# Kernel optimization log

Hardware: AMD Instinct MI355X
Metric: run time of the kernel (lower is better)

The kernel has to match this reference:

```python
import jax, jax.numpy as jnp
import numpy as np

D_MODEL = 1024
H = 16
D_K = D_MODEL // H
EPS = 1e-8


def _feature_map(x):
    # elu(x) + 1 (Performer/linear-attention positive feature map)
    return jax.nn.elu(x) + 1.0


def setup_inputs() -> dict:
    key = jax.random.key(0)
    ks = jax.random.split(key, 8)
    B, L = 4, 2048
    q = jax.random.normal(ks[0], (B, L, D_MODEL), dtype=jnp.float32)
    k = jax.random.normal(ks[1], (B, L, D_MODEL), dtype=jnp.float32)
    v = jax.random.normal(ks[2], (B, L, D_MODEL), dtype=jnp.float32)
    mask = jnp.ones((B, 1, 1, L), dtype=bool)
    s = 1.0 / np.sqrt(D_MODEL)
    w_q = jax.random.normal(ks[3], (D_MODEL, D_MODEL), dtype=jnp.float32) * s
    w_k = jax.random.normal(ks[4], (D_MODEL, D_MODEL), dtype=jnp.float32) * s
    w_v = jax.random.normal(ks[5], (D_MODEL, D_MODEL), dtype=jnp.float32) * s
    w_o = jax.random.normal(ks[6], (D_MODEL, D_MODEL), dtype=jnp.float32) * s
    return {"q": q, "k": k, "v": v, "mask": mask,
            "w_q": w_q, "w_k": w_k, "w_v": w_v, "w_o": w_o}


def reference(q, k, v, mask, w_q, w_k, w_v, w_o):
    # Linear (use_Linear=True) branch of MultiHeadAttentionBlock.forward.
    B, Lq, _ = q.shape
    Lk = k.shape[1]
    # fused-style projections (torch Linear: x @ W.T), split into heads -> bhnd
    query = (q @ w_q.T).reshape(B, Lq, H, D_K).transpose(0, 2, 1, 3)
    key_  = (k @ w_k.T).reshape(B, Lk, H, D_K).transpose(0, 2, 1, 3)
    value = (v @ w_v.T).reshape(B, Lk, H, D_K).transpose(0, 2, 1, 3)

    Q = _feature_map(query)            # [B,H,Lq,d_k]
    K = _feature_map(key_)             # [B,H,Lk,d_k]
    KV = jnp.einsum('bhnd,bhnm->bhdm', K, value)           # [B,H,d_k,d_k]
    Z = 1.0 / (jnp.einsum('bhnd,bhd->bhn', Q, K.sum(axis=2)) + EPS)  # [B,H,Lq]
    out = jnp.einsum('bhnd,bhdm,bhn->bhnm', Q, KV, Z)      # [B,H,Lq,d_k]

    out = out.transpose(0, 2, 1, 3).reshape(B, Lq, D_MODEL)
    return out @ w_o.T
```

## Files before the change

### kernel.cpp

```cpp
#include <hip/hip_runtime.h>
#include <cstdint>
#include <cstddef>

typedef __bf16 bf16;
typedef __bf16 bf16x8 __attribute__((ext_vector_type(8)));
typedef __bf16 bf16x4 __attribute__((ext_vector_type(4)));
typedef float  f32x4  __attribute__((ext_vector_type(4)));

#define DM     1024
#define MROWS  8192
#define LSEQ   2048
#define NHEAD  16
#define BHEADS 64
#define KV_S   16
#define KVT_STRIDE 4160

__device__ __forceinline__ void async16(const void* g, void* l) {
    __builtin_amdgcn_global_load_lds(
        (const __attribute__((address_space(1))) void*)g,
        (__attribute__((address_space(3))) void*)l, 16, 0, 0);
}

struct CastArgs {
    const float* s[7];
    bf16*        d[7];
    int          n4[7];
};

__global__ __launch_bounds__(256) void cast_all(CastArgs a) {
    const int z = blockIdx.z;
    const int n4 = a.n4[z];
    const float* __restrict__ s = a.s[z];
    bf16* __restrict__ d = a.d[z];
    for (int i = blockIdx.x * 256 + threadIdx.x; i < n4; i += 1024 * 256) {
        float4 f = ((const float4*)s)[i];
        bf16x4 o; o[0] = (bf16)f.x; o[1] = (bf16)f.y; o[2] = (bf16)f.z; o[3] = (bf16)f.w;
        ((bf16x4*)d)[i] = o;
    }
}

struct GemmArgs {
    const bf16* A[3];
    const bf16* B[3];
    void*       C[3];
    int         mode[3];
};

__global__ __launch_bounds__(256, 3) void gemm_nt(GemmArgs args) {
    const int z = blockIdx.z;
    const bf16* __restrict__ A  = args.A[z];
    const bf16* __restrict__ Bm = args.B[z];
    void* Cp = args.C[z];
    const int mode = args.mode[z];
    const int K = DM;

    __shared__ __attribute__((aligned(16))) bf16 sA[128 * 64];
    __shared__ __attribute__((aligned(16))) bf16 sB[128 * 64];

    const int tid  = threadIdx.x;
    const int wave = tid >> 6;
    const int lane = tid & 63;
    const int wm = wave >> 1, wn = wave & 1;

    const int fb = blockIdx.x + 8 * (int)blockIdx.y;
    const int bx = (fb >> 3) & 7;
    const int by = (fb & 7) * 8 + (fb >> 6);
    const int row0 = by * 128;
    const int col0 = bx * 128;

    const int rr = lane >> 3;
    const int cc = lane & 7;
    const int csw = ((cc ^ rr) * 8);
    const bf16* gA = A  + (size_t)(row0 + wave * 32 + rr) * K + csw;
    const bf16* gB = Bm + (size_t)(col0 + wave * 32 + rr) * K + csw;

    f32x4 acc[4][4] = {};

    const int lr = lane & 15;
    const int qd = lane >> 4;
    const int swz = lr & 7;

    for (int k0 = 0; k0 < K; k0 += 64) {
        #pragma unroll
        for (int j = 0; j < 4; ++j) {
            async16(gA + k0 + (size_t)(j * 8) * K, &sA[(wave * 32 + j * 8) * 64]);
            async16(gB + k0 + (size_t)(j * 8) * K, &sB[(wave * 32 + j * 8) * 64]);
        }
        __syncthreads();

        #pragma unroll
        for (int ks = 0; ks < 2; ++ks) {
            bf16x8 af[4], bfr[4];
            #pragma unroll
            for (int mi = 0; mi < 4; ++mi)
                af[mi] = *(const bf16x8*)&sA[(wm * 64 + mi * 16 + lr) * 64 + (((ks * 4 + qd) ^ swz) * 8)];
            #pragma unroll
            for (int ni = 0; ni < 4; ++ni)
                bfr[ni] = *(const bf16x8*)&sB[(wn * 64 + ni * 16 + lr) * 64 + (((ks * 4 + qd) ^ swz) * 8)];
            #pragma unroll
            for (int mi = 0; mi < 4; ++mi)
                #pragma unroll
                for (int ni = 0; ni < 4; ++ni)
                    acc[mi][ni] = __builtin_amdgcn_mfma_f32_16x16x32_bf16(af[mi], bfr[ni], acc[mi][ni], 0, 0, 0);
        }
        __syncthreads();
    }

    if (mode >= 3) {
        #pragma unroll
        for (int mi = 0; mi < 4; ++mi) {
            const int grow0 = row0 + wm * 64 + mi * 16 + qd * 4;
            const int b  = grow0 >> 11;
            const int n0 = grow0 & 2047;
            #pragma unroll
            for (int ni = 0; ni < 4; ++ni) {
                const int gcol = col0 + wn * 64 + ni * 16 + lr;
                const int h = gcol >> 6;
                const int d = gcol & 63;
                bf16x4 o;
                #pragma unroll
                for (int r = 0; r < 4; ++r) {
                    float val = acc[mi][ni][r];
                    if (mode == 4) val = (val > 0.f) ? (val + 1.f) : __expf(val);
                    o[r] = (bf16)val;
                }
                *(bf16x4*)&((bf16*)Cp)[(size_t)((b * 16 + h) * 64 + d) * 2048 + n0] = o;
            }
        }
    } else {
        #pragma unroll
        for (int mi = 0; mi < 4; ++mi) {
            #pragma unroll
            for (int ni = 0; ni < 4; ++ni) {
                #pragma unroll
                for (int r = 0; r < 4; ++r) {
                    const int grow = row0 + wm * 64 + mi * 16 + qd * 4 + r;
                    const int gcol = col0 + wn * 64 + ni * 16 + lr;
                    float val = acc[mi][ni][r];
                    if (mode == 1) val = (val > 0.f) ? (val + 1.f) : __expf(val);
                    ((bf16*)Cp)[(size_t)grow * DM + gcol] = (bf16)val;
                }
            }
        }
    }
}

__global__ __launch_bounds__(256, 4) void gemm_fin(const bf16* __restrict__ A,
                                                   const bf16* __restrict__ Bm,
                                                   float* __restrict__ C) {
    const int K = DM;
    __shared__ __attribute__((aligned(16))) bf16 sA[128 * 64];
    __shared__ __attribute__((aligned(16))) bf16 sB[64 * 64];

    const int tid  = threadIdx.x;
    const int wave = tid >> 6;
    const int lane = tid & 63;
    const int wm = wave >> 1, wn = wave & 1;

    const int fb = blockIdx.x + 16 * (int)blockIdx.y;
    const int xcd = fb & 7;
    const int g = fb >> 3;
    const int bx = g & 15;
    const int by = xcd * 8 + (g >> 4);
    const int row0 = by * 128;
    const int col0 = bx * 64;

    const int rr = lane >> 3;
    const int cc = lane & 7;
    const int csw = ((cc ^ rr) * 8);
    const bf16* gA = A  + (size_t)(row0 + wave * 32 + rr) * K + csw;
    const bf16* gB = Bm + (size_t)(col0 + wave * 16 + rr) * K + csw;

    f32x4 acc[4][2] = {};

    const int lr = lane & 15;
    const int qd = lane >> 4;
    const int swz = lr & 7;

    for (int k0 = 0; k0 < K; k0 += 64) {
        #pragma unroll
        for (int j = 0; j < 4; ++j)
            async16(gA + k0 + (size_t)(j * 8) * K, &sA[(wave * 32 + j * 8) * 64]);
        #pragma unroll
        for (int j = 0; j < 2; ++j)
            async16(gB + k0 + (size_t)(j * 8) * K, &sB[(wave * 16 + j * 8) * 64]);
        __syncthreads();

        #pragma unroll
        for (int ks = 0; ks < 2; ++ks) {
            bf16x8 af[4], bfr[2];
            #pragma unroll
            for (int mi = 0; mi < 4; ++mi)
                af[mi] = *(const bf16x8*)&sA[(wm * 64 + mi * 16 + lr) * 64 + (((ks * 4 + qd) ^ swz) * 8)];
            #pragma unroll
            for (int ni = 0; ni < 2; ++ni)
                bfr[ni] = *(const bf16x8*)&sB[(wn * 32 + ni * 16 + lr) * 64 + (((ks * 4 + qd) ^ swz) * 8)];
            #pragma unroll
            for (int mi = 0; mi < 4; ++mi)
                #pragma unroll
                for (int ni = 0; ni < 2; ++ni)
                    acc[mi][ni] = __builtin_amdgcn_mfma_f32_16x16x32_bf16(af[mi], bfr[ni], acc[mi][ni], 0, 0, 0);
        }
        __syncthreads();
    }

    #pragma unroll
    for (int mi = 0; mi < 4; ++mi)
        #pragma unroll
        for (int ni = 0; ni < 2; ++ni)
            #pragma unroll
            for (int r = 0; r < 4; ++r) {
                const int grow = row0 + wm * 64 + mi * 16 + qd * 4 + r;
                const int gcol = col0 + wn * 32 + ni * 16 + lr;
                C[(size_t)grow * DM + gcol] = acc[mi][ni][r];
            }
}

__global__ __launch_bounds__(256, 4) void kv_mfma(const bf16* __restrict__ KpT,
                                                  const bf16* __restrict__ VpT,
                                                  float* __restrict__ KVTp) {
    const int bh = blockIdx.x, s = blockIdx.y;
    const int tid = threadIdx.x, wave = tid >> 6, lane = tid & 63;

    __shared__ __attribute__((aligned(16))) bf16 sVT[64 * 128];
    __shared__ __attribute__((aligned(16))) bf16 sKT[64 * 128];

    #pragma unroll
    for (int j = 0; j < 4; ++j) {
        const int r  = wave * 16 + j * 4 + (lane >> 4);
        const int cg = (lane & 15) ^ (r & 7);
        const size_t gofs = (size_t)(bh * 64 + r) * 2048 + s * 128 + cg * 8;
        async16(VpT + gofs, &sVT[(wave * 16 + j * 4) * 128]);
        async16(KpT + gofs, &sKT[(wave * 16 + j * 4) * 128]);
    }
    __syncthreads();

    const int lr = lane & 15, qd = lane >> 4;
    f32x4 acc[4] = {};
    const int rA = wave * 16 + lr;
    #pragma unroll
    for (int k0 = 0; k0 < 4; ++k0) {
        const int ch = k0 * 4 + qd;
        bf16x8 a = *(const bf16x8*)&sVT[rA * 128 + ((ch ^ (rA & 7)) * 8)];
        #pragma unroll
        for (int ni = 0; ni < 4; ++ni) {
            const int rB = ni * 16 + lr;
            bf16x8 b = *(const bf16x8*)&sKT[rB * 128 + ((ch ^ (rB & 7)) * 8)];
            acc[ni] = __builtin_amdgcn_mfma_f32_16x16x32_bf16(a, b, acc[ni], 0, 0, 0);
        }
    }

    float* outp = &KVTp[(size_t)(bh * KV_S + s) * KVT_STRIDE];
    #pragma unroll
    for (int ni = 0; ni < 4; ++ni)
        #pragma unroll
        for (int r = 0; r < 4; ++r)
            outp[(wave * 16 + qd * 4 + r) * 64 + ni * 16 + lr] = acc[ni][r];

    if (wave == 0) {
        float ks = 0.f;
        #pragma unroll
        for (int c2 = 0; c2 < 16; ++c2) {
            bf16x8 kk = *(const bf16x8*)&sKT[lane * 128 + ((c2 ^ (lane & 7)) * 8)];
            #pragma unroll
            for (int j = 0; j < 8; ++j) ks += (float)kk[j];
        }
        outp[4096 + lane] = ks;
    }
}

__global__ __launch_bounds__(256) void kv_reduce(const float* __restrict__ KVTp,
                                                 bf16* __restrict__ KVT,
                                                 float* __restrict__ Ksum) {
    const int bh = blockIdx.x;
    const int idx = blockIdx.y * 256 + threadIdx.x;
    if (idx >= KVT_STRIDE) return;
    float s = 0.f;
    #pragma unroll
    for (int p = 0; p < KV_S; ++p) s += KVTp[(size_t)(bh * KV_S + p) * KVT_STRIDE + idx];
    if (idx < 4096) KVT[(size_t)bh * 4096 + idx] = (bf16)s;
    else            Ksum[bh * 64 + (idx - 4096)] = s;
}

__global__ __launch_bounds__(256, 4) void attn_out(const bf16* __restrict__ Qp,
                                                   const bf16* __restrict__ KVT,
                                                   const float* __restrict__ Ksum,
                                                   bf16* __restrict__ Ab) {
    const int bh = blockIdx.y;
    const int b = bh >> 4, h = bh & 15;
    const int row0 = blockIdx.x * 128;
    const int tid = threadIdx.x, wave = tid >> 6, lane = tid & 63;

    __shared__ __attribute__((aligned(16))) bf16 sQ[128 * 64];
    __shared__ __attribute__((aligned(16))) bf16 sKV[64 * 64];
    __shared__ float sKs[64];

    const int rr8 = lane >> 3;
    const int cc8 = lane & 7;
    const int csw = ((cc8 ^ rr8) * 8);

    const bf16* qbase = &Qp[(size_t)(b * LSEQ + row0) * DM + h * 64];
    #pragma unroll
    for (int j = 0; j < 4; ++j) {
        const int r0 = wave * 32 + j * 8;
        async16(qbase + (size_t)(r0 + rr8) * DM + csw, &sQ[r0 * 64]);
    }
    const bf16* kvbase = &KVT[(size_t)bh * 4096];
    #pragma unroll
    for (int j = 0; j < 2; ++j) {
        const int r0 = wave * 16 + j * 8;
        async16(kvbase + (r0 + rr8) * 64 + csw, &sKV[r0 * 64]);
    }
    if (tid < 64) sKs[tid] = Ksum[bh * 64 + tid];
    __syncthreads();

    const int zrow = lane >> 1;
    const int dh = lane & 1;
    float zacc = 0.f;
    {
        const bf16* qr = &sQ[(wave * 32 + zrow) * 64];
        #pragma unroll
        for (int c = 0; c < 4; ++c) {
            const int chunk = dh * 4 + c;
            bf16x8 q8 = *(const bf16x8*)&qr[(chunk ^ (zrow & 7)) * 8];
            const float* ksp = &sKs[chunk * 8];
            #pragma unroll
            for (int j = 0; j < 8; ++j) zacc += (float)q8[j] * ksp[j];
        }
    }
    zacc += __shfl_xor(zacc, 1, 64);
    const float zinv = 1.0f / (zacc + 1e-8f);

    f32x4 acc[2][4] = {};
    const int lr = lane & 15, qd = lane >> 4;
    const int swz = lr & 7;
    #pragma unroll
    for (int ks = 0; ks < 2; ++ks) {
        bf16x8 af[2], bfr[4];
        #pragma unroll
        for (int mi = 0; mi < 2; ++mi)
            af[mi] = *(const bf16x8*)&sQ[(wave * 32 + mi * 16 + lr) * 64 + (((ks * 4 + qd) ^ swz) * 8)];
        #pragma unroll
        for (int ni = 0; ni < 4; ++ni)
            bfr[ni] = *(const bf16x8*)&sKV[(ni * 16 + lr) * 64 + (((ks * 4 + qd) ^ swz) * 8)];
        #pragma unroll
        for (int mi = 0; mi < 2; ++mi)
            #pragma unroll
            for (int ni = 0; ni < 4; ++ni)
                acc[mi][ni] = __builtin_amdgcn_mfma_f32_16x16x32_bf16(af[mi], bfr[ni], acc[mi][ni], 0, 0, 0);
    }

    #pragma unroll
    for (int mi = 0; mi < 2; ++mi) {
        #pragma unroll
        for (int rr = 0; rr < 4; ++rr) {
            const int rlocal = mi * 16 + qd * 4 + rr;
            const float zv = __shfl(zinv, rlocal * 2, 64);
            const int nrow = row0 + wave * 32 + rlocal;
            #pragma unroll
            for (int ni = 0; ni < 4; ++ni)
                Ab[(size_t)(b * LSEQ + nrow) * DM + h * 64 + ni * 16 + lr] =
                    (bf16)(acc[mi][ni][rr] * zv);
        }
    }
}

extern "C" void kernel_launch(void* const* d_in, const int* in_sizes, int n_in,
                              void* d_out, int out_size, void* d_ws, size_t ws_size,
                              hipStream_t stream) {
    const float* q  = (const float*)d_in[0];
    const float* k  = (const float*)d_in[1];
    const float* v  = (const float*)d_in[2];
    const float* wq = (const float*)d_in[4];
    const float* wk = (const float*)d_in[5];
    const float* wv = (const float*)d_in[6];
    const float* wo = (const float*)d_in[7];

    char* ws = (char*)d_ws;
    size_t off = 0;
    auto alloc = [&](size_t bytes) -> void* {
        void* p = ws + off;
        off += (bytes + 255) & ~(size_t)255;
        return p;
    };

    bf16* qb   = (bf16*)alloc((size_t)MROWS * DM * 2);
    bf16* kb   = (bf16*)alloc((size_t)MROWS * DM * 2);
    bf16* vb   = (bf16*)alloc((size_t)MROWS * DM * 2);
    bf16* wqb  = (bf16*)alloc((size_t)DM * DM * 2);
    bf16* wkb  = (bf16*)alloc((size_t)DM * DM * 2);
    bf16* wvb  = (bf16*)alloc((size_t)DM * DM * 2);
    bf16* wob  = (bf16*)alloc((size_t)DM * DM * 2);
    bf16* Qp   = (bf16*)alloc((size_t)MROWS * DM * 2);
    bf16* KpT  = (bf16*)alloc((size_t)MROWS * DM * 2);
    bf16* VpT  = (bf16*)alloc((size_t)MROWS * DM * 2);
    bf16* Ab   = (bf16*)alloc((size_t)MROWS * DM * 2);
    float* KVTp = (float*)alloc((size_t)BHEADS * KV_S * KVT_STRIDE * 4);
    bf16* KVT  = (bf16*)alloc((size_t)BHEADS * 4096 * 2);
    float* Ksum = (float*)alloc((size_t)BHEADS * 64 * 4);

    CastArgs ca;
    ca.s[0] = q;  ca.s[1] = k;  ca.s[2] = v;  ca.s[3] = wq; ca.s[4] = wk; ca.s[5] = wv; ca.s[6] = wo;
    ca.d[0] = qb; ca.d[1] = kb; ca.d[2] = vb; ca.d[3] = wqb; ca.d[4] = wkb; ca.d[5] = wvb; ca.d[6] = wob;
    const int n4_big = MROWS * DM / 4, n4_w = DM * DM / 4;
    ca.n4[0] = n4_big; ca.n4[1] = n4_big; ca.n4[2] = n4_big;
    ca.n4[3] = n4_w; ca.n4[4] = n4_w; ca.n4[5] = n4_w; ca.n4[6] = n4_w;
    cast_all<<<dim3(1024, 1, 7), 256, 0, stream>>>(ca);

    GemmArgs pa;
    pa.A[0] = qb;  pa.A[1] = kb;  pa.A[2] = vb;
    pa.B[0] = wqb; pa.B[1] = wkb; pa.B[2] = wvb;
    pa.C[0] = Qp;  pa.C[1] = KpT; pa.C[2] = VpT;
    pa.mode[0] = 1; pa.mode[1] = 4; pa.mode[2] = 3;
    gemm_nt<<<dim3(DM / 128, MROWS / 128, 3), 256, 0, stream>>>(pa);

    kv_mfma<<<dim3(BHEADS, KV_S), 256, 0, stream>>>(KpT, VpT, KVTp);
    kv_reduce<<<dim3(BHEADS, (KVT_STRIDE + 255) / 256), 256, 0, stream>>>(KVTp, KVT, Ksum);

    attn_out<<<dim3(LSEQ / 128, BHEADS), 256, 0, stream>>>(Qp, KVT, Ksum, Ab);

    gemm_fin<<<dim3(DM / 64, MROWS / 128), 256, 0, stream>>>(Ab, wob, (float*)d_out);
}
```

Before: 256.6 us.

## Fuse fp32-to-bf16 activation cast into projection GEMM and enlarge output GEMM tile

```diff
diff --git a/kernel.cpp b/kernel.cpp
--- a/kernel.cpp
+++ b/kernel.cpp
@@ -22,40 +22,35 @@
 }
 
 struct CastArgs {
-    const float* s[7];
-    bf16*        d[7];
-    int          n4[7];
+    const float* s[4];
+    bf16*        d[4];
 };
 
-__global__ __launch_bounds__(256) void cast_all(CastArgs a) {
+__global__ __launch_bounds__(256) void cast_w(CastArgs a) {
     const int z = blockIdx.z;
-    const int n4 = a.n4[z];
-    const float* __restrict__ s = a.s[z];
-    bf16* __restrict__ d = a.d[z];
-    for (int i = blockIdx.x * 256 + threadIdx.x; i < n4; i += 1024 * 256) {
-        float4 f = ((const float4*)s)[i];
-        bf16x4 o; o[0] = (bf16)f.x; o[1] = (bf16)f.y; o[2] = (bf16)f.z; o[3] = (bf16)f.w;
-        ((bf16x4*)d)[i] = o;
-    }
+    const int i = blockIdx.x * 256 + threadIdx.x;
+    float4 f = ((const float4*)a.s[z])[i];
+    bf16x4 o; o[0] = (bf16)f.x; o[1] = (bf16)f.y; o[2] = (bf16)f.z; o[3] = (bf16)f.w;
+    ((bf16x4*)a.d[z])[i] = o;
 }
 
 struct GemmArgs {
-    const bf16* A[3];
-    const bf16* B[3];
-    void*       C[3];
-    int         mode[3];
+    const float* A[3];
+    const bf16*  B[3];
+    void*        C[3];
+    int          mode[3];
 };
 
 __global__ __launch_bounds__(256, 3) void gemm_nt(GemmArgs args) {
     const int z = blockIdx.z;
-    const bf16* __restrict__ A  = args.A[z];
-    const bf16* __restrict__ Bm = args.B[z];
+    const float* __restrict__ A  = args.A[z];
+    const bf16*  __restrict__ Bm = args.B[z];
     void* Cp = args.C[z];
     const int mode = args.mode[z];
     const int K = DM;
 
-    __shared__ __attribute__((aligned(16))) bf16 sA[128 * 64];
-    __shared__ __attribute__((aligned(16))) bf16 sB[128 * 64];
+    __shared__ __attribute__((aligned(16))) float sAf[128 * 64];
+    __shared__ __attribute__((aligned(16))) bf16  sB[128 * 64];
 
     const int tid  = threadIdx.x;
     const int wave = tid >> 6;
@@ -68,11 +63,12 @@
     const int row0 = by * 128;
     const int col0 = bx * 128;
 
-    const int rr = lane >> 3;
-    const int cc = lane & 7;
-    const int csw = ((cc ^ rr) * 8);
-    const bf16* gA = A  + (size_t)(row0 + wave * 32 + rr) * K + csw;
-    const bf16* gB = Bm + (size_t)(col0 + wave * 32 + rr) * K + csw;
+    const int rr4  = lane >> 4;
+    const int cc16 = lane & 15;
+    const int rr8 = lane >> 3;
+    const int cc8 = lane & 7;
+    const int cswB = ((cc8 ^ rr8) * 8);
+    const bf16* gB = Bm + (size_t)(col0 + wave * 32 + rr8) * K + cswB;
 
     f32x4 acc[4][4] = {};
 
@@ -82,18 +78,30 @@
 
     for (int k0 = 0; k0 < K; k0 += 64) {
         #pragma unroll
-        for (int j = 0; j < 4; ++j) {
-            async16(gA + k0 + (size_t)(j * 8) * K, &sA[(wave * 32 + j * 8) * 64]);
+        for (int j = 0; j < 8; ++j) {
+            const int rl = wave * 32 + j * 4 + rr4;
+            const int g  = cc16 ^ (rl & 7);
+            async16(A + (size_t)(row0 + rl) * K + k0 + g * 4, &sAf[(wave * 32 + j * 4) * 64]);
+        }
+        #pragma unroll
+        for (int j = 0; j < 4; ++j)
             async16(gB + k0 + (size_t)(j * 8) * K, &sB[(wave * 32 + j * 8) * 64]);
-        }
         __syncthreads();
 
         #pragma unroll
         for (int ks = 0; ks < 2; ++ks) {
             bf16x8 af[4], bfr[4];
             #pragma unroll
-            for (int mi = 0; mi < 4; ++mi)
-                af[mi] = *(const bf16x8*)&sA[(wm * 64 + mi * 16 + lr) * 64 + (((ks * 4 + qd) ^ swz) * 8)];
+            for (int mi = 0; mi < 4; ++mi) {
+                const int row = wm * 64 + mi * 16 + lr;
+                const int c0 = (ks * 4 + qd) * 2;
+                f32x4 lo = *(const f32x4*)&sAf[row * 64 + ((c0 ^ swz) * 4)];
+                f32x4 hi = *(const f32x4*)&sAf[row * 64 + (((c0 + 1) ^ swz) * 4)];
+                bf16x8 t;
+                t[0] = (bf16)lo[0]; t[1] = (bf16)lo[1]; t[2] = (bf16)lo[2]; t[3] = (bf16)lo[3];
+                t[4] = (bf16)hi[0]; t[5] = (bf16)hi[1]; t[6] = (bf16)hi[2]; t[7] = (bf16)hi[3];
+                af[mi] = t;
+            }
             #pragma unroll
             for (int ni = 0; ni < 4; ++ni)
                 bfr[ni] = *(const bf16x8*)&sB[(wn * 64 + ni * 16 + lr) * 64 + (((ks * 4 + qd) ^ swz) * 8)];
@@ -145,33 +153,31 @@
     }
 }
 
-__global__ __launch_bounds__(256, 4) void gemm_fin(const bf16* __restrict__ A,
+__global__ __launch_bounds__(256, 3) void gemm_fin(const bf16* __restrict__ A,
                                                    const bf16* __restrict__ Bm,
                                                    float* __restrict__ C) {
     const int K = DM;
     __shared__ __attribute__((aligned(16))) bf16 sA[128 * 64];
-    __shared__ __attribute__((aligned(16))) bf16 sB[64 * 64];
+    __shared__ __attribute__((aligned(16))) bf16 sB[128 * 64];
 
     const int tid  = threadIdx.x;
     const int wave = tid >> 6;
     const int lane = tid & 63;
     const int wm = wave >> 1, wn = wave & 1;
 
-    const int fb = blockIdx.x + 16 * (int)blockIdx.y;
-    const int xcd = fb & 7;
-    const int g = fb >> 3;
-    const int bx = g & 15;
-    const int by = xcd * 8 + (g >> 4);
+    const int fb = blockIdx.x + 8 * (int)blockIdx.y;
+    const int bx = (fb >> 3) & 7;
+    const int by = (fb & 7) * 8 + (fb >> 6);
     const int row0 = by * 128;
-    const int col0 = bx * 64;
+    const int col0 = bx * 128;
 
     const int rr = lane >> 3;
     const int cc = lane & 7;
     const int csw = ((cc ^ rr) * 8);
     const bf16* gA = A  + (size_t)(row0 + wave * 32 + rr) * K + csw;
-    const bf16* gB = Bm + (size_t)(col0 + wave * 16 + rr) * K + csw;
-
-    f32x4 acc[4][2] = {};
+    const bf16* gB = Bm + (size_t)(col0 + wave * 32 + rr) * K + csw;
+
+    f32x4 acc[4][4] = {};
 
     const int lr = lane & 15;
     const int qd = lane >> 4;
@@ -179,26 +185,25 @@
 
     for (int k0 = 0; k0 < K; k0 += 64) {
         #pragma unroll
-        for (int j = 0; j < 4; ++j)
+        for (int j = 0; j < 4; ++j) {
             async16(gA + k0 + (size_t)(j * 8) * K, &sA[(wave * 32 + j * 8) * 64]);
-        #pragma unroll
-        for (int j = 0; j < 2; ++j)
-            async16(gB + k0 + (size_t)(j * 8) * K, &sB[(wave * 16 + j * 8) * 64]);
+            async16(gB + k0 + (size_t)(j * 8) * K, &sB[(wave * 32 + j * 8) * 64]);
+        }
         __syncthreads();
 
         #pragma unroll
         for (int ks = 0; ks < 2; ++ks) {
-            bf16x8 af[4], bfr[2];
+            bf16x8 af[4], bfr[4];
             #pragma unroll
             for (int mi = 0; mi < 4; ++mi)
                 af[mi] = *(const bf16x8*)&sA[(wm * 64 + mi * 16 + lr) * 64 + (((ks * 4 + qd) ^ swz) * 8)];
             #pragma unroll
-            for (int ni = 0; ni < 2; ++ni)
-                bfr[ni] = *(const bf16x8*)&sB[(wn * 32 + ni * 16 + lr) * 64 + (((ks * 4 + qd) ^ swz) * 8)];
+            for (int ni = 0; ni < 4; ++ni)
+                bfr[ni] = *(const bf16x8*)&sB[(wn * 64 + ni * 16 + lr) * 64 + (((ks * 4 + qd) ^ swz) * 8)];
             #pragma unroll
             for (int mi = 0; mi < 4; ++mi)
                 #pragma unroll
-                for (int ni = 0; ni < 2; ++ni)
+                for (int ni = 0; ni < 4; ++ni)
                     acc[mi][ni] = __builtin_amdgcn_mfma_f32_16x16x32_bf16(af[mi], bfr[ni], acc[mi][ni], 0, 0, 0);
         }
         __syncthreads();
@@ -207,11 +212,11 @@
     #pragma unroll
     for (int mi = 0; mi < 4; ++mi)
         #pragma unroll
-        for (int ni = 0; ni < 2; ++ni)
+        for (int ni = 0; ni < 4; ++ni)
             #pragma unroll
             for (int r = 0; r < 4; ++r) {
                 const int grow = row0 + wm * 64 + mi * 16 + qd * 4 + r;
-                const int gcol = col0 + wn * 32 + ni * 16 + lr;
+                const int gcol = col0 + wn * 64 + ni * 16 + lr;
                 C[(size_t)grow * DM + gcol] = acc[mi][ni][r];
             }
 }
@@ -384,9 +389,6 @@
         return p;
     };
 
-    bf16* qb   = (bf16*)alloc((size_t)MROWS * DM * 2);
-    bf16* kb   = (bf16*)alloc((size_t)MROWS * DM * 2);
-    bf16* vb   = (bf16*)alloc((size_t)MROWS * DM * 2);
     bf16* wqb  = (bf16*)alloc((size_t)DM * DM * 2);
     bf16* wkb  = (bf16*)alloc((size_t)DM * DM * 2);
     bf16* wvb  = (bf16*)alloc((size_t)DM * DM * 2);
@@ -400,15 +402,12 @@
     float* Ksum = (float*)alloc((size_t)BHEADS * 64 * 4);
 
     CastArgs ca;
-    ca.s[0] = q;  ca.s[1] = k;  ca.s[2] = v;  ca.s[3] = wq; ca.s[4] = wk; ca.s[5] = wv; ca.s[6] = wo;
-    ca.d[0] = qb; ca.d[1] = kb; ca.d[2] = vb; ca.d[3] = wqb; ca.d[4] = wkb; ca.d[5] = wvb; ca.d[6] = wob;
-    const int n4_big = MROWS * DM / 4, n4_w = DM * DM / 4;
-    ca.n4[0] = n4_big; ca.n4[1] = n4_big; ca.n4[2] = n4_big;
-    ca.n4[3] = n4_w; ca.n4[4] = n4_w; ca.n4[5] = n4_w; ca.n4[6] = n4_w;
-    cast_all<<<dim3(1024, 1, 7), 256, 0, stream>>>(ca);
+    ca.s[0] = wq;  ca.s[1] = wk;  ca.s[2] = wv;  ca.s[3] = wo;
+    ca.d[0] = wqb; ca.d[1] = wkb; ca.d[2] = wvb; ca.d[3] = wob;
+    cast_w<<<dim3(DM * DM / 4 / 256, 1, 4), 256, 0, stream>>>(ca);
 
     GemmArgs pa;
-    pa.A[0] = qb;  pa.A[1] = kb;  pa.A[2] = vb;
+    pa.A[0] = q;   pa.A[1] = k;   pa.A[2] = v;
     pa.B[0] = wqb; pa.B[1] = wkb; pa.B[2] = wvb;
     pa.C[0] = Qp;  pa.C[1] = KpT; pa.C[2] = VpT;
     pa.mode[0] = 1; pa.mode[1] = 4; pa.mode[2] = 3;
@@ -419,5 +418,5 @@
 
     attn_out<<<dim3(LSEQ / 128, BHEADS), 256, 0, stream>>>(Qp, KVT, Ksum, Ab);
 
-    gemm_fin<<<dim3(DM / 64, MROWS / 128), 256, 0, stream>>>(Ab, wob, (float*)d_out);
-}
+    gemm_fin<<<dim3(DM / 128, MROWS / 128), 256, 0, stream>>>(Ab, wob, (float*)d_out);
+}
```

Result: slower. 269.5 us (+5.0%).

## Enlarge output GEMM tile to 128x128 and halve KV split partials in bf16

Applied to the files above, without the earlier changes.

```diff
diff --git a/kernel.cpp b/kernel.cpp
--- a/kernel.cpp
+++ b/kernel.cpp
@@ -12,8 +12,7 @@
 #define LSEQ   2048
 #define NHEAD  16
 #define BHEADS 64
-#define KV_S   16
-#define KVT_STRIDE 4160
+#define KV_S   8
 
 __device__ __forceinline__ void async16(const void* g, void* l) {
     __builtin_amdgcn_global_load_lds(
@@ -145,33 +144,31 @@
     }
 }
 
-__global__ __launch_bounds__(256, 4) void gemm_fin(const bf16* __restrict__ A,
+__global__ __launch_bounds__(256, 3) void gemm_fin(const bf16* __restrict__ A,
                                                    const bf16* __restrict__ Bm,
                                                    float* __restrict__ C) {
     const int K = DM;
     __shared__ __attribute__((aligned(16))) bf16 sA[128 * 64];
-    __shared__ __attribute__((aligned(16))) bf16 sB[64 * 64];
+    __shared__ __attribute__((aligned(16))) bf16 sB[128 * 64];
 
     const int tid  = threadIdx.x;
     const int wave = tid >> 6;
     const int lane = tid & 63;
     const int wm = wave >> 1, wn = wave & 1;
 
-    const int fb = blockIdx.x + 16 * (int)blockIdx.y;
-    const int xcd = fb & 7;
-    const int g = fb >> 3;
-    const int bx = g & 15;
-    const int by = xcd * 8 + (g >> 4);
+    const int fb = blockIdx.x + 8 * (int)blockIdx.y;
+    const int bx = (fb >> 3) & 7;
+    const int by = (fb & 7) * 8 + (fb >> 6);
     const int row0 = by * 128;
-    const int col0 = bx * 64;
+    const int col0 = bx * 128;
 
     const int rr = lane >> 3;
     const int cc = lane & 7;
     const int csw = ((cc ^ rr) * 8);
     const bf16* gA = A  + (size_t)(row0 + wave * 32 + rr) * K + csw;
-    const bf16* gB = Bm + (size_t)(col0 + wave * 16 + rr) * K + csw;
-
-    f32x4 acc[4][2] = {};
+    const bf16* gB = Bm + (size_t)(col0 + wave * 32 + rr) * K + csw;
+
+    f32x4 acc[4][4] = {};
 
     const int lr = lane & 15;
     const int qd = lane >> 4;
@@ -179,26 +176,25 @@
 
     for (int k0 = 0; k0 < K; k0 += 64) {
         #pragma unroll
-        for (int j = 0; j < 4; ++j)
+        for (int j = 0; j < 4; ++j) {
             async16(gA + k0 + (size_t)(j * 8) * K, &sA[(wave * 32 + j * 8) * 64]);
-        #pragma unroll
-        for (int j = 0; j < 2; ++j)
-            async16(gB + k0 + (size_t)(j * 8) * K, &sB[(wave * 16 + j * 8) * 64]);
+            async16(gB + k0 + (size_t)(j * 8) * K, &sB[(wave * 32 + j * 8) * 64]);
+        }
         __syncthreads();
 
         #pragma unroll
         for (int ks = 0; ks < 2; ++ks) {
-            bf16x8 af[4], bfr[2];
+            bf16x8 af[4], bfr[4];
             #pragma unroll
             for (int mi = 0; mi < 4; ++mi)
                 af[mi] = *(const bf16x8*)&sA[(wm * 64 + mi * 16 + lr) * 64 + (((ks * 4 + qd) ^ swz) * 8)];
             #pragma unroll
-            for (int ni = 0; ni < 2; ++ni)
-                bfr[ni] = *(const bf16x8*)&sB[(wn * 32 + ni * 16 + lr) * 64 + (((ks * 4 + qd) ^ swz) * 8)];
+            for (int ni = 0; ni < 4; ++ni)
+                bfr[ni] = *(const bf16x8*)&sB[(wn * 64 + ni * 16 + lr) * 64 + (((ks * 4 + qd) ^ swz) * 8)];
             #pragma unroll
             for (int mi = 0; mi < 4; ++mi)
                 #pragma unroll
-                for (int ni = 0; ni < 2; ++ni)
+                for (int ni = 0; ni < 4; ++ni)
                     acc[mi][ni] = __builtin_amdgcn_mfma_f32_16x16x32_bf16(af[mi], bfr[ni], acc[mi][ni], 0, 0, 0);
         }
         __syncthreads();
@@ -207,79 +203,91 @@
     #pragma unroll
     for (int mi = 0; mi < 4; ++mi)
         #pragma unroll
-        for (int ni = 0; ni < 2; ++ni)
+        for (int ni = 0; ni < 4; ++ni)
             #pragma unroll
             for (int r = 0; r < 4; ++r) {
                 const int grow = row0 + wm * 64 + mi * 16 + qd * 4 + r;
-                const int gcol = col0 + wn * 32 + ni * 16 + lr;
+                const int gcol = col0 + wn * 64 + ni * 16 + lr;
                 C[(size_t)grow * DM + gcol] = acc[mi][ni][r];
             }
 }
 
 __global__ __launch_bounds__(256, 4) void kv_mfma(const bf16* __restrict__ KpT,
                                                   const bf16* __restrict__ VpT,
-                                                  float* __restrict__ KVTp) {
+                                                  bf16* __restrict__ KVTp,
+                                                  float* __restrict__ KsumP) {
     const int bh = blockIdx.x, s = blockIdx.y;
     const int tid = threadIdx.x, wave = tid >> 6, lane = tid & 63;
 
     __shared__ __attribute__((aligned(16))) bf16 sVT[64 * 128];
     __shared__ __attribute__((aligned(16))) bf16 sKT[64 * 128];
 
-    #pragma unroll
-    for (int j = 0; j < 4; ++j) {
-        const int r  = wave * 16 + j * 4 + (lane >> 4);
-        const int cg = (lane & 15) ^ (r & 7);
-        const size_t gofs = (size_t)(bh * 64 + r) * 2048 + s * 128 + cg * 8;
-        async16(VpT + gofs, &sVT[(wave * 16 + j * 4) * 128]);
-        async16(KpT + gofs, &sKT[(wave * 16 + j * 4) * 128]);
-    }
-    __syncthreads();
-
     const int lr = lane & 15, qd = lane >> 4;
     f32x4 acc[4] = {};
+    float ks = 0.f;
     const int rA = wave * 16 + lr;
-    #pragma unroll
-    for (int k0 = 0; k0 < 4; ++k0) {
-        const int ch = k0 * 4 + qd;
-        bf16x8 a = *(const bf16x8*)&sVT[rA * 128 + ((ch ^ (rA & 7)) * 8)];
-        #pragma unroll
-        for (int ni = 0; ni < 4; ++ni) {
-            const int rB = ni * 16 + lr;
-            bf16x8 b = *(const bf16x8*)&sKT[rB * 128 + ((ch ^ (rB & 7)) * 8)];
-            acc[ni] = __builtin_amdgcn_mfma_f32_16x16x32_bf16(a, b, acc[ni], 0, 0, 0);
-        }
-    }
-
-    float* outp = &KVTp[(size_t)(bh * KV_S + s) * KVT_STRIDE];
+
+    #pragma unroll
+    for (int sub = 0; sub < 2; ++sub) {
+        #pragma unroll
+        for (int j = 0; j < 4; ++j) {
+            const int r  = wave * 16 + j * 4 + (lane >> 4);
+            const int cg = (lane & 15) ^ (r & 7);
+            const size_t gofs = (size_t)(bh * 64 + r) * 2048 + (s * 2 + sub) * 128 + cg * 8;
+            async16(VpT + gofs, &sVT[(wave * 16 + j * 4) * 128]);
+            async16(KpT + gofs, &sKT[(wave * 16 + j * 4) * 128]);
+        }
+        __syncthreads();
+
+        #pragma unroll
+        for (int k0 = 0; k0 < 4; ++k0) {
+            const int ch = k0 * 4 + qd;
+            bf16x8 a = *(const bf16x8*)&sVT[rA * 128 + ((ch ^ (rA & 7)) * 8)];
+            #pragma unroll
+            for (int ni = 0; ni < 4; ++ni) {
+                const int rB = ni * 16 + lr;
+                bf16x8 b = *(const bf16x8*)&sKT[rB * 128 + ((ch ^ (rB & 7)) * 8)];
+                acc[ni] = __builtin_amdgcn_mfma_f32_16x16x32_bf16(a, b, acc[ni], 0, 0, 0);
+            }
+        }
+        if (wave == 0) {
+            #pragma unroll
+            for (int c2 = 0; c2 < 16; ++c2) {
+                bf16x8 kk = *(const bf16x8*)&sKT[lane * 128 + ((c2 ^ (lane & 7)) * 8)];
+                #pragma unroll
+                for (int j = 0; j < 8; ++j) ks += (float)kk[j];
+            }
+        }
+        __syncthreads();
+    }
+
+    bf16* outp = &KVTp[(size_t)(bh * KV_S + s) * 4096];
     #pragma unroll
     for (int ni = 0; ni < 4; ++ni)
         #pragma unroll
         for (int r = 0; r < 4; ++r)
-            outp[(wave * 16 + qd * 4 + r) * 64 + ni * 16 + lr] = acc[ni][r];
-
-    if (wave == 0) {
-        float ks = 0.f;
-        #pragma unroll
-        for (int c2 = 0; c2 < 16; ++c2) {
-            bf16x8 kk = *(const bf16x8*)&sKT[lane * 128 + ((c2 ^ (lane & 7)) * 8)];
-            #pragma unroll
-            for (int j = 0; j < 8; ++j) ks += (float)kk[j];
-        }
-        outp[4096 + lane] = ks;
-    }
-}
-
-__global__ __launch_bounds__(256) void kv_reduce(const float* __restrict__ KVTp,
+            outp[(wave * 16 + qd * 4 + r) * 64 + ni * 16 + lr] = (bf16)acc[ni][r];
+
+    if (wave == 0) KsumP[(bh * KV_S + s) * 64 + lane] = ks;
+}
+
+__global__ __launch_bounds__(256) void kv_reduce(const bf16* __restrict__ KVTp,
+                                                 const float* __restrict__ KsumP,
                                                  bf16* __restrict__ KVT,
                                                  float* __restrict__ Ksum) {
     const int bh = blockIdx.x;
-    const int idx = blockIdx.y * 256 + threadIdx.x;
-    if (idx >= KVT_STRIDE) return;
-    float s = 0.f;
-    #pragma unroll
-    for (int p = 0; p < KV_S; ++p) s += KVTp[(size_t)(bh * KV_S + p) * KVT_STRIDE + idx];
-    if (idx < 4096) KVT[(size_t)bh * 4096 + idx] = (bf16)s;
-    else            Ksum[bh * 64 + (idx - 4096)] = s;
+    if (blockIdx.y < 16) {
+        const int idx = blockIdx.y * 256 + threadIdx.x;
+        float s = 0.f;
+        #pragma unroll
+        for (int p = 0; p < KV_S; ++p) s += (float)KVTp[(size_t)(bh * KV_S + p) * 4096 + idx];
+        KVT[(size_t)bh * 4096 + idx] = (bf16)s;
+    } else if (threadIdx.x < 64) {
+        float s = 0.f;
+        #pragma unroll
+        for (int p = 0; p < KV_S; ++p) s += KsumP[(bh * KV_S + p) * 64 + threadIdx.x];
+        Ksum[bh * 64 + threadIdx.x] = s;
+    }
 }
 
 __global__ __launch_bounds__(256, 4) void attn_out(const bf16* __restrict__ Qp,
@@ -395,7 +403,8 @@
     bf16* KpT  = (bf16*)alloc((size_t)MROWS * DM * 2);
     bf16* VpT  = (bf16*)alloc((size_t)MROWS * DM * 2);
     bf16* Ab   = (bf16*)alloc((size_t)MROWS * DM * 2);
-    float* KVTp = (float*)alloc((size_t)BHEADS * KV_S * KVT_STRIDE * 4);
+    bf16* KVTp = (bf16*)alloc((size_t)BHEADS * KV_S * 4096 * 2);
+    float* KsumP = (float*)alloc((size_t)BHEADS * KV_S * 64 * 4);
     bf16* KVT  = (bf16*)alloc((size_t)BHEADS * 4096 * 2);
     float* Ksum = (float*)alloc((size_t)BHEADS * 64 * 4);
 
@@ -414,10 +423,10 @@
     pa.mode[0] = 1; pa.mode[1] = 4; pa.mode[2] = 3;
     gemm_nt<<<dim3(DM / 128, MROWS / 128, 3), 256, 0, stream>>>(pa);
 
-    kv_mfma<<<dim3(BHEADS, KV_S), 256, 0, stream>>>(KpT, VpT, KVTp);
-    kv_reduce<<<dim3(BHEADS, (KVT_STRIDE + 255) / 256), 256, 0, stream>>>(KVTp, KVT, Ksum);
+    kv_mfma<<<dim3(BHEADS, KV_S), 256, 0, stream>>>(KpT, VpT, KVTp, KsumP);
+    kv_reduce<<<dim3(BHEADS, 17), 256, 0, stream>>>(KVTp, KsumP, KVT, Ksum);
 
     attn_out<<<dim3(LSEQ / 128, BHEADS), 256, 0, stream>>>(Qp, KVT, Ksum, Ab);
 
-    gemm_fin<<<dim3(DM / 64, MROWS / 128), 256, 0, stream>>>(Ab, wob, (float*)d_out);
-}
+    gemm_fin<<<dim3(DM / 128, MROWS / 128), 256, 0, stream>>>(Ab, wob, (float*)d_out);
+}
```

New measurement: 258.4 us. No clear change (+0.7%).
